# Optimization experiments

Measured on AMD Instinct MI355X. Metric: run time of the kernel, lower is better.

Reference implementation:

```python
import jax, jax.numpy as jnp
import numpy as np

N_EMBD = 1024
H_DIM = 1024
NB = 16          # blocks resolved by _find_dynamic_num_blocks for all projections
N_MEM = 128
N_FORG = H_DIM - N_MEM
RANK = 64
LOG_DT_INIT = -2.0
EPS = 1.1920929e-07  # torch fp32 finfo eps used by F.rms_norm


def rms_norm(x):
    return x * jax.lax.rsqrt(jnp.mean(jnp.square(x), axis=-1, keepdims=True) + EPS)


def silu(x):
    return x * jax.nn.sigmoid(x)


def blockdiag(x, w):
    # x: [..., nb*bi], w: [nb, bo, bi] -> [..., nb*bo]
    nb, bo, bi = w.shape
    xs = x.reshape(*x.shape[:-1], nb, bi)
    y = jnp.einsum('...ni,noi->...no', xs, w)
    return y.reshape(*x.shape[:-1], nb * bo)


def causal_scan(drive, a):
    # drive: [B,T,D] float32, a: [D] per-channel decay; causal conv with kernel a^t via FFT
    B, T, D = drive.shape
    steps = jnp.arange(T, dtype=jnp.float32)
    kernel = jnp.exp(jnp.log(jnp.maximum(a, 1e-6))[:, None] * steps[None, :])  # [D,T]
    n_fft = 1 << int(2 * T - 1).bit_length()
    df = jnp.fft.rfft(drive.astype(jnp.float32).transpose(0, 2, 1), n=n_fft, axis=-1)
    kf = jnp.fft.rfft(kernel, n=n_fft, axis=-1)
    y = jnp.fft.irfft(df * kf[None], n=n_fft, axis=-1)[..., :T]
    return y.transpose(0, 2, 1).astype(drive.dtype)


def geom_gain(a, K):
    one_minus = 1.0 - a
    safe = jnp.maximum(one_minus, 1e-8)
    return jnp.where(jnp.abs(one_minus) < 1e-6,
                     jnp.full_like(a, float(K)),
                     (1.0 - a ** K) / safe)


def setup_inputs() -> dict:
    key = jax.random.key(0)
    ks = jax.random.split(key, 10)
    s = 0.02
    bi_e, bo_h = N_EMBD // NB, H_DIM // NB
    bi_p = (2 * N_EMBD + H_DIM) // NB
    bo_e = N_EMBD // NB
    return {
        'x': jax.random.normal(ks[0], (4, 4096, N_EMBD), dtype=jnp.float32),
        'active_k': 4,
        'b_seq_w': jax.random.normal(ks[1], (NB, bo_h, bi_e), jnp.float32) * s,
        'b_depth_w': jax.random.normal(ks[2], (NB, bo_h, bi_e), jnp.float32) * s,
        'w_post_w': jax.random.normal(ks[3], (NB, bo_h, bi_p), jnp.float32) * s,
        'w_local_w': jax.random.normal(ks[4], (NB, bo_e, H_DIM // NB), jnp.float32) * s,
        'lr_A': jax.random.normal(ks[5], (N_EMBD, RANK), jnp.float32) * s,
        'lr_B': jax.random.normal(ks[6], (RANK, H_DIM), jnp.float32) * s,
        'log_A_seq': jnp.zeros((H_DIM,), jnp.float32),
        'log_dt_seq': jnp.full((H_DIM,), LOG_DT_INIT, jnp.float32),
        'log_A_depth': jnp.zeros((N_FORG,), jnp.float32),
        'log_dt_depth': jnp.full((N_FORG,), LOG_DT_INIT, jnp.float32),
    }


def reference(x, active_k, b_seq_w, b_depth_w, w_post_w, w_local_w, lr_A, lr_B,
              log_A_seq, log_dt_seq, log_A_depth, log_dt_depth):
    K = int(active_k)
    e = rms_norm(x)
    shifted_e = jnp.pad(e[:, :-1], ((0, 0), (1, 0), (0, 0)))
    a_seq = jnp.exp(-jnp.exp(log_A_seq) * jnp.exp(log_dt_seq))
    h_seq = causal_scan(silu(blockdiag(e, b_seq_w)), a_seq)
    a_forg = jnp.exp(-jnp.exp(log_A_depth) * jnp.exp(log_dt_depth))
    a_depth = jnp.concatenate([jnp.ones((N_MEM,), a_forg.dtype), a_forg], axis=0)
    gain = geom_gain(a_depth, K).astype(x.dtype)
    h_depth = gain * silu(blockdiag(e, b_depth_w))
    h = h_seq + h_depth
    r = silu(blockdiag(jnp.concatenate([rms_norm(h), e, shifted_e], axis=-1), w_post_w))
    out = x + blockdiag(r, w_local_w) + (r @ lr_B.T) @ lr_A.T
    return out
```

## Files before the change

kernel.cpp:

```cpp
#include <hip/hip_runtime.h>

#define B_ 4
#define T_ 4096
#define D_ 1024
#define R_ (B_*T_)
#define CHUNK_ 64
#define NCH_ (T_/CHUNK_)
#define EPS_ 1.1920929e-07f

typedef unsigned short ushort_t;
typedef __attribute__((ext_vector_type(8))) short short8;
typedef __attribute__((ext_vector_type(4))) float f32x4;

__device__ __forceinline__ float silu_f(float v){ return v / (1.0f + __expf(-v)); }

__device__ __forceinline__ ushort_t f2bf(float f){
    unsigned u = __float_as_uint(f);
    unsigned r = u + 0x7fffu + ((u>>16)&1u);
    return (ushort_t)(r>>16);
}
__device__ __forceinline__ float bf2f(ushort_t s){ return __uint_as_float(((unsigned)s)<<16); }

__device__ __forceinline__ f32x4 mfma16(short8 a, short8 b, f32x4 c){
    return __builtin_amdgcn_mfma_f32_16x16x32_bf16(a, b, c, 0, 0, 0);
}

__global__ void prep_k(const float* __restrict__ s0, const float* __restrict__ s1,
                       const float* __restrict__ s2, const float* __restrict__ s3,
                       const float* __restrict__ s4, const float* __restrict__ s5,
                       ushort_t* __restrict__ d0, ushort_t* __restrict__ d1,
                       ushort_t* __restrict__ d2, ushort_t* __restrict__ d3,
                       ushort_t* __restrict__ d4, ushort_t* __restrict__ d5,
                       const float* __restrict__ logA_seq, const float* __restrict__ logdt_seq,
                       const float* __restrict__ logA_dep, const float* __restrict__ logdt_dep,
                       const int* __restrict__ active_k,
                       float* __restrict__ aseq, float* __restrict__ apowC,
                       float* __restrict__ gain, float* __restrict__ apowtab){
    int i = blockIdx.x*256 + threadIdx.x;
    if      (i < 65536)   d0[i] = f2bf(s0[i]);
    else if (i < 131072)  d1[i-65536] = f2bf(s1[i-65536]);
    else if (i < 327680)  d2[i-131072] = f2bf(s2[i-131072]);
    else if (i < 393216)  d3[i-327680] = f2bf(s3[i-327680]);
    else if (i < 458752)  d4[i-393216] = f2bf(s4[i-393216]);
    else if (i < 524288)  d5[i-458752] = f2bf(s5[i-458752]);
    else if (i < 524288 + D_){
        int d = i - 524288;
        float K = (float)(*active_k);
        float a = expf(-expf(logA_seq[d]) * expf(logdt_seq[d]));
        a = fmaxf(a, 1e-6f);
        aseq[d] = a;
        apowC[d] = powf(a, (float)CHUNK_);
        float ap = a;
        for (int s2=0;s2<CHUNK_;++s2){ apowtab[s2*D_ + d] = ap; ap *= a; }
        float g;
        if (d < 128) {
            g = K;
        } else {
            float ad = expf(-expf(logA_dep[d-128]) * expf(logdt_dep[d-128]));
            float om = 1.0f - ad;
            if (fabsf(om) < 1e-6f) g = K;
            else g = (1.0f - powf(ad, K)) / fmaxf(om, 1e-8f);
        }
        gain[d] = g;
    }
}

__global__ __launch_bounds__(256) void rmsbf_k(const float* __restrict__ x, ushort_t* __restrict__ e){
    int row = blockIdx.x;
    int tid = threadIdx.x;
    float4 v = ((const float4*)(x + (size_t)row*D_))[tid];
    float ss = v.x*v.x + v.y*v.y + v.z*v.z + v.w*v.w;
    for (int off=32; off; off>>=1) ss += __shfl_down(ss, off, 64);
    __shared__ float red[4];
    if ((tid&63)==0) red[tid>>6] = ss;
    __syncthreads();
    float tot = red[0]+red[1]+red[2]+red[3];
    float scale = 1.0f / sqrtf(tot*(1.0f/D_) + EPS_);
    ushort4 o;
    o.x = f2bf(v.x*scale); o.y = f2bf(v.y*scale); o.z = f2bf(v.z*scale); o.w = f2bf(v.w*scale);
    ((ushort4*)(e + (size_t)row*D_))[tid] = o;
}

__global__ __launch_bounds__(256) void bd2s_k(const ushort_t* __restrict__ e,
        const ushort_t* __restrict__ wseq, const ushort_t* __restrict__ wdep,
        const float* __restrict__ gain, const float* __restrict__ aseq,
        ushort_t* __restrict__ hsum, float* __restrict__ carry){
    __shared__ __align__(16) ushort_t st[4][16][72];
    int wave = threadIdx.x>>6, lane = threadIdx.x&63;
    int m = lane&15, quad = lane>>4;
    int orow = lane>>2, oq = lane&3;
    int n = blockIdx.y;
    int chunk0 = blockIdx.x*256 + wave*64;

    short8 bs[2][4], bd[2][4];
    #pragma unroll
    for (int s=0;s<2;++s)
        #pragma unroll
        for (int c=0;c<4;++c){
            bs[s][c] = *(const short8*)(wseq + n*4096 + (c*16+m)*64 + s*32 + quad*8);
            bd[s][c] = *(const short8*)(wdep + n*4096 + (c*16+m)*64 + s*32 + quad*8);
        }
    float g[4], av[4], a4v[4], C[4];
    #pragma unroll
    for (int c=0;c<4;++c){
        g[c]  = gain[n*64 + c*16 + m];
        float a = aseq[n*64 + c*16 + m];
        av[c] = a;
        float a2 = a*a;
        a4v[c] = a2*a2;
        C[c] = 0.f;
    }

    #pragma unroll
    for (int t=0;t<4;++t){
        int r0 = chunk0 + t*16;
        const ushort_t* ab = e + (size_t)(r0+m)*D_ + n*64 + quad*8;
        short8 a0 = *(const short8*)ab;
        short8 a1 = *(const short8*)(ab + 32);
        f32x4 accs[4], accd[4];
        #pragma unroll
        for (int c=0;c<4;++c){
            accs[c]=(f32x4)0.f; accd[c]=(f32x4)0.f;
            accs[c]=mfma16(a0, bs[0][c], accs[c]);
            accd[c]=mfma16(a0, bd[0][c], accd[c]);
            accs[c]=mfma16(a1, bs[1][c], accs[c]);
            accd[c]=mfma16(a1, bd[1][c], accd[c]);
        }
        #pragma unroll
        for (int c=0;c<4;++c){
            float a  = av[c];
            float d0 = silu_f(accs[c][0]);
            float d1 = silu_f(accs[c][1]);
            float d2 = silu_f(accs[c][2]);
            float d3 = silu_f(accs[c][3]);
            float p1 = fmaf(a, d0, d1);
            float p2 = fmaf(a, p1, d2);
            float p3 = fmaf(a, p2, d3);
            float M = a4v[c], Bv = p3;
            float Mp = __shfl_up(M, 16, 64);
            float Bp = __shfl_up(Bv, 16, 64);
            if (quad >= 1){ Bv = fmaf(M, Bp, Bv); M *= Mp; }
            Mp = __shfl_up(M, 32, 64);
            Bp = __shfl_up(Bv, 32, 64);
            if (quad >= 2){ Bv = fmaf(M, Bp, Bv); M *= Mp; }
            float KB = __shfl_up(Bv, 16, 64);
            float KM = __shfl_up(M, 16, 64);
            float K  = (quad==0) ? C[c] : fmaf(KM, C[c], KB);
            float h0 = fmaf(a, K,  d0);
            float h1 = fmaf(a, h0, d1);
            float h2 = fmaf(a, h1, d2);
            float h3 = fmaf(a, h2, d3);
            float Cn = fmaf(M, C[c], Bv);
            C[c] = __shfl(Cn, 48 + m, 64);
            st[wave][quad*4+0][c*16+m] = f2bf(h0 + g[c]*silu_f(accd[c][0]));
            st[wave][quad*4+1][c*16+m] = f2bf(h1 + g[c]*silu_f(accd[c][1]));
            st[wave][quad*4+2][c*16+m] = f2bf(h2 + g[c]*silu_f(accd[c][2]));
            st[wave][quad*4+3][c*16+m] = f2bf(h3 + g[c]*silu_f(accd[c][3]));
        }
        ushort_t* db = hsum + (size_t)(r0+orow)*D_ + n*64;
        #pragma unroll
        for (int it=0;it<2;++it)
            *(short8*)(db + (it*4+oq)*8) = *(const short8*)&st[wave][orow][(it*4+oq)*8];
    }
    float Cv = (quad==0) ? C[0] : (quad==1) ? C[1] : (quad==2) ? C[2] : C[3];
    carry[(size_t)(chunk0>>6)*D_ + n*64 + lane] = Cv;
}

__global__ __launch_bounds__(64) void scan2_k(float* __restrict__ carry, const float* __restrict__ apowC){
    int tid = blockIdx.x*64 + threadIdx.x;
    int d = tid & (D_-1);
    int b = tid >> 10;
    float aC = apowC[d];
    float s[NCH_];
    #pragma unroll
    for (int c=0;c<NCH_;++c) s[c] = carry[(size_t)(b*NCH_+c)*D_ + d];
    float pref = 0.f;
    #pragma unroll
    for (int c=0;c<NCH_;++c){
        float cur = s[c];
        carry[(size_t)(b*NCH_+c)*D_ + d] = pref;
        pref = fmaf(aC, pref, cur);
    }
}

__global__ __launch_bounds__(256) void scan3s_k(const ushort_t* __restrict__ hsum,
                                                const float* __restrict__ aseq,
                                                const float* __restrict__ carry,
                                                const float* __restrict__ apowtab,
                                                ushort_t* __restrict__ hn){
    __shared__ float part[4][4];
    __shared__ float scl[8];
    int tid = threadIdx.x;
    int lane = tid & 63, wave = tid >> 6;
    int cg = tid & 127;
    int rp = tid >> 7;
    int d0 = cg*8;
    int row0 = blockIdx.x*8;
    int bc = row0 >> 6;
    int s0 = row0 & 63;

    float a2[8], P[8], apow[8];
    #pragma unroll
    for (int j=0;j<8;++j){
        float aj = aseq[d0+j];
        a2[j] = aj*aj;
        P[j]  = carry[(size_t)bc*D_ + d0 + j];
        apow[j] = apowtab[(size_t)(s0 + rp)*D_ + d0 + j];
    }

    float hf[4][8];
    #pragma unroll
    for (int i=0;i<4;++i){
        int row = row0 + i*2 + rp;
        short8 v = *(const short8*)(hsum + (size_t)row*D_ + d0);
        float ss = 0.f;
        #pragma unroll
        for (int j=0;j<8;++j){
            float f = bf2f((ushort_t)v[j]) + P[j]*apow[j];
            hf[i][j] = f;
            ss += f*f;
            apow[j] *= a2[j];
        }
        for (int off=32; off; off>>=1) ss += __shfl_down(ss, off, 64);
        if (lane==0) part[wave][i] = ss;
    }
    __syncthreads();
    if (tid < 8){
        int r = tid;
        int rr = r & 1, ii = r >> 1;
        float sum = part[rr*2][ii] + part[rr*2+1][ii];
        scl[r] = rsqrtf(sum*(1.0f/D_) + EPS_);
    }
    __syncthreads();
    #pragma unroll
    for (int i=0;i<4;++i){
        int rloc = i*2 + rp;
        float sc = scl[rloc];
        short8 o;
        #pragma unroll
        for (int j=0;j<8;++j) o[j] = (short)f2bf(hf[i][j]*sc);
        *(short8*)(hn + (size_t)(row0 + rloc)*D_ + d0) = o;
    }
}

__global__ __launch_bounds__(256) void post_k(const ushort_t* __restrict__ hn,
                                              const ushort_t* __restrict__ e,
                                              const ushort_t* __restrict__ wpost, ushort_t* __restrict__ rout){
    __shared__ __align__(16) ushort_t st[4][16][72];
    int wave = threadIdx.x>>6, lane = threadIdx.x&63;
    int m = lane&15, quad = lane>>4;
    int orow = lane>>2, oq = lane&3;
    int n = blockIdx.y;
    int row0 = blockIdx.x*128 + wave*32 + m;

    f32x4 acc[2][4];
    #pragma unroll
    for (int t=0;t<2;++t)
        #pragma unroll
        for (int c=0;c<4;++c) acc[t][c]=(f32x4)0.f;

    #pragma unroll 1
    for (int s=0;s<6;++s){
        int g0 = n*192 + s*32;
        short8 bw[4];
        #pragma unroll
        for (int c=0;c<4;++c)
            bw[c] = *(const short8*)(wpost + n*(64*192) + (c*16+m)*192 + s*32 + quad*8);
        #pragma unroll
        for (int t=0;t<2;++t){
            int row = row0 + t*16;
            short8 af;
            if (g0 < 1024){
                af = *(const short8*)(hn + (size_t)row*D_ + g0 + quad*8);
            } else if (g0 < 2048){
                af = *(const short8*)(e + (size_t)row*D_ + (g0-1024) + quad*8);
            } else {
                if ((row & (T_-1)) == 0) af = short8{0,0,0,0,0,0,0,0};
                else af = *(const short8*)(e + (size_t)(row-1)*D_ + (g0-2048) + quad*8);
            }
            #pragma unroll
            for (int c=0;c<4;++c)
                acc[t][c] = mfma16(af, bw[c], acc[t][c]);
        }
    }
    #pragma unroll
    for (int t=0;t<2;++t){
        int r0 = blockIdx.x*128 + wave*32 + t*16;
        #pragma unroll
        for (int c=0;c<4;++c)
            #pragma unroll
            for (int r=0;r<4;++r)
                st[wave][quad*4+r][c*16+m] = f2bf(silu_f(acc[t][c][r]));
        ushort_t* db = rout + (size_t)(r0+orow)*D_ + n*64;
        #pragma unroll
        for (int it=0;it<2;++it)
            *(short8*)(db + (it*4+oq)*8) = *(const short8*)&st[wave][orow][(it*4+oq)*8];
    }
}

__global__ __launch_bounds__(256) void rlow_k(const ushort_t* __restrict__ r, const ushort_t* __restrict__ lrB,
                                              ushort_t* __restrict__ rlow){
    __shared__ __align__(16) float sacc[4][16][68];
    int wave = threadIdx.x>>6, lane = threadIdx.x&63;
    int m = lane&15, quad = lane>>4;
    int r0 = blockIdx.x*16;
    f32x4 acc[4];
    #pragma unroll
    for (int c=0;c<4;++c) acc[c]=(f32x4)0.f;
    const ushort_t* ab = r + (size_t)(r0+m)*D_ + wave*256 + quad*8;
    #pragma unroll
    for (int s=0;s<8;++s){
        short8 a = *(const short8*)(ab + s*32);
        #pragma unroll
        for (int c=0;c<4;++c){
            short8 b = *(const short8*)(lrB + (c*16+m)*1024 + wave*256 + s*32 + quad*8);
            acc[c] = mfma16(a, b, acc[c]);
        }
    }
    #pragma unroll
    for (int c=0;c<4;++c)
        #pragma unroll
        for (int r2=0;r2<4;++r2)
            sacc[wave][quad*4+r2][c*16+m] = acc[c][r2];
    __syncthreads();
    int row  = threadIdx.x>>4;
    int col4 = (threadIdx.x&15)*4;
    float4 v0 = *(const float4*)&sacc[0][row][col4];
    float4 v1 = *(const float4*)&sacc[1][row][col4];
    float4 v2 = *(const float4*)&sacc[2][row][col4];
    float4 v3 = *(const float4*)&sacc[3][row][col4];
    ushort4 o;
    o.x = f2bf(v0.x+v1.x+v2.x+v3.x);
    o.y = f2bf(v0.y+v1.y+v2.y+v3.y);
    o.z = f2bf(v0.z+v1.z+v2.z+v3.z);
    o.w = f2bf(v0.w+v1.w+v2.w+v3.w);
    *(ushort4*)(rlow + (size_t)(r0+row)*64 + col4) = o;
}

__global__ __launch_bounds__(256) void out_k(const float* __restrict__ x, const ushort_t* __restrict__ r,
        const ushort_t* __restrict__ rlow, const ushort_t* __restrict__ wloc, const ushort_t* __restrict__ lrA,
        float* __restrict__ out){
    __shared__ __align__(16) float st[4][16][68];
    int wave = threadIdx.x>>6, lane = threadIdx.x&63;
    int m = lane&15, quad = lane>>4;
    int orow = lane>>2, oq = lane&3;
    int n = blockIdx.y;

    short8 wl[2][4], la[4][2];
    #pragma unroll
    for (int c=0;c<4;++c)
        #pragma unroll
        for (int s=0;s<2;++s){
            wl[s][c] = *(const short8*)(wloc + n*4096 + (c*16+m)*64 + s*32 + quad*8);
            la[c][s] = *(const short8*)(lrA + (size_t)(n*64 + c*16 + m)*64 + s*32 + quad*8);
        }
    #pragma unroll
    for (int t=0;t<2;++t){
        int r0 = blockIdx.x*128 + wave*32 + t*16;
        const float* xb = x + (size_t)(r0+orow)*D_ + n*64;
        float4 xv[4];
        #pragma unroll
        for (int it=0;it<4;++it) xv[it] = *(const float4*)(xb + (it*4+oq)*4);

        const ushort_t* lb = rlow + (size_t)(r0+m)*64 + quad*8;
        short8 al0 = *(const short8*)lb;
        short8 al1 = *(const short8*)(lb + 32);
        const ushort_t* ab = r + (size_t)(r0+m)*D_ + n*64 + quad*8;
        short8 ar0 = *(const short8*)ab;
        short8 ar1 = *(const short8*)(ab + 32);
        f32x4 acc[4];
        #pragma unroll
        for (int c=0;c<4;++c){
            acc[c]=(f32x4)0.f;
            acc[c]=mfma16(al0, la[c][0], acc[c]);
            acc[c]=mfma16(al1, la[c][1], acc[c]);
            acc[c]=mfma16(ar0, wl[0][c], acc[c]);
            acc[c]=mfma16(ar1, wl[1][c], acc[c]);
        }
        #pragma unroll
        for (int c=0;c<4;++c)
            #pragma unroll
            for (int r2=0;r2<4;++r2)
                st[wave][quad*4+r2][c*16+m] = acc[c][r2];
        float* ob = out + (size_t)(r0+orow)*D_ + n*64;
        #pragma unroll
        for (int it=0;it<4;++it){
            float4 v = *(const float4*)&st[wave][orow][(it*4+oq)*4];
            v.x += xv[it].x; v.y += xv[it].y; v.z += xv[it].z; v.w += xv[it].w;
            *(float4*)(ob + (it*4+oq)*4) = v;
        }
    }
}

extern "C" void kernel_launch(void* const* d_in, const int* in_sizes, int n_in,
                              void* d_out, int out_size, void* d_ws, size_t ws_size,
                              hipStream_t stream) {
    const float* x         = (const float*)d_in[0];
    const int*   active_k  = (const int*)  d_in[1];
    const float* b_seq_w   = (const float*)d_in[2];
    const float* b_depth_w = (const float*)d_in[3];
    const float* w_post_w  = (const float*)d_in[4];
    const float* w_local_w = (const float*)d_in[5];
    const float* lr_A      = (const float*)d_in[6];
    const float* lr_B      = (const float*)d_in[7];
    const float* logA_seq  = (const float*)d_in[8];
    const float* logdt_seq = (const float*)d_in[9];
    const float* logA_dep  = (const float*)d_in[10];
    const float* logdt_dep = (const float*)d_in[11];

    float* ws      = (float*)d_ws;
    float* carry   = ws;
    float* aseq    = carry + (size_t)B_*NCH_*D_;
    float* apowC   = aseq + D_;
    float* gain    = apowC + D_;
    float* apowtab = gain + D_;
    ushort_t* ub       = (ushort_t*)(apowtab + (size_t)CHUNK_*D_);
    ushort_t* e_bf     = ub;
    ushort_t* hsum_bf  = e_bf + (size_t)R_*D_;
    ushort_t* hn_bf    = hsum_bf + (size_t)R_*D_;
    ushort_t* r_bf     = hn_bf + (size_t)R_*D_;
    ushort_t* rlow_bf  = r_bf + (size_t)R_*D_;
    ushort_t* wseq_bf  = rlow_bf + (size_t)R_*64;
    ushort_t* wdep_bf  = wseq_bf + 65536;
    ushort_t* wpost_bf = wdep_bf + 65536;
    ushort_t* wloc_bf  = wpost_bf + 196608;
    ushort_t* lrA_bf   = wloc_bf + 65536;
    ushort_t* lrB_bf   = lrA_bf + 65536;

    prep_k<<<(524288 + D_ + 255)/256, 256, 0, stream>>>(
        b_seq_w, b_depth_w, w_post_w, w_local_w, lr_A, lr_B,
        wseq_bf, wdep_bf, wpost_bf, wloc_bf, lrA_bf, lrB_bf,
        logA_seq, logdt_seq, logA_dep, logdt_dep, active_k, aseq, apowC, gain, apowtab);

    rmsbf_k <<<R_, 256, 0, stream>>>(x, e_bf);
    bd2s_k  <<<dim3(R_/256, 16), 256, 0, stream>>>(e_bf, wseq_bf, wdep_bf, gain, aseq,
                                                   hsum_bf, carry);
    scan2_k <<<(B_*D_)/64, 64, 0, stream>>>(carry, apowC);
    scan3s_k<<<R_/8, 256, 0, stream>>>(hsum_bf, aseq, carry, apowtab, hn_bf);
    post_k  <<<dim3(R_/128, 16), 256, 0, stream>>>(hn_bf, e_bf, wpost_bf, r_bf);
    rlow_k  <<<R_/16, 256, 0, stream>>>(r_bf, lrB_bf, rlow_bf);
    out_k   <<<dim3(R_/128, 16), 256, 0, stream>>>(x, r_bf, rlow_bf, wloc_bf, lrA_bf, (float*)d_out);
}
```

Baseline: 271.3 us.

## Stage post_k weights in LDS and prefetch activations via global_load_lds

```diff
diff --git a/kernel.cpp b/kernel.cpp
--- a/kernel.cpp
+++ b/kernel.cpp
@@ -11,6 +11,8 @@
 typedef unsigned short ushort_t;
 typedef __attribute__((ext_vector_type(8))) short short8;
 typedef __attribute__((ext_vector_type(4))) float f32x4;
+typedef __attribute__((address_space(1))) ushort_t gu16;
+typedef __attribute__((address_space(3))) ushort_t lu16;
 
 __device__ __forceinline__ float silu_f(float v){ return v / (1.0f + __expf(-v)); }
 
@@ -246,38 +248,66 @@
 __global__ __launch_bounds__(256) void post_k(const ushort_t* __restrict__ hn,
                                               const ushort_t* __restrict__ e,
                                               const ushort_t* __restrict__ wpost, ushort_t* __restrict__ rout){
-    __shared__ __align__(16) ushort_t st[4][16][72];
+    __shared__ __align__(16) ushort_t stage[4][6144];
+    __shared__ __align__(16) ushort_t wlds[64*208];
     int wave = threadIdx.x>>6, lane = threadIdx.x&63;
     int m = lane&15, quad = lane>>4;
     int orow = lane>>2, oq = lane&3;
     int n = blockIdx.y;
     int row0 = blockIdx.x*128 + wave*32 + m;
-
-    f32x4 acc[2][4];
-    #pragma unroll
-    for (int t=0;t<2;++t)
-        #pragma unroll
-        for (int c=0;c<4;++c) acc[t][c]=(f32x4)0.f;
-
-    #pragma unroll 1
+    ushort_t* wst = &stage[wave][0];
+
+    {
+        const ushort_t* wsrc = wpost + n*(64*192);
+        int tid = threadIdx.x;
+        #pragma unroll
+        for (int k=0;k<6;++k){
+            int chunk = tid + k*256;
+            int rr = chunk / 24, cc = chunk % 24;
+            *(short8*)(wlds + rr*208 + cc*8) = *(const short8*)(wsrc + rr*192 + cc*8);
+        }
+    }
+    __syncthreads();
+
+    #pragma unroll
     for (int s=0;s<6;++s){
         int g0 = n*192 + s*32;
-        short8 bw[4];
-        #pragma unroll
-        for (int c=0;c<4;++c)
-            bw[c] = *(const short8*)(wpost + n*(64*192) + (c*16+m)*192 + s*32 + quad*8);
         #pragma unroll
         for (int t=0;t<2;++t){
             int row = row0 + t*16;
-            short8 af;
-            if (g0 < 1024){
-                af = *(const short8*)(hn + (size_t)row*D_ + g0 + quad*8);
-            } else if (g0 < 2048){
-                af = *(const short8*)(e + (size_t)row*D_ + (g0-1024) + quad*8);
-            } else {
-                if ((row & (T_-1)) == 0) af = short8{0,0,0,0,0,0,0,0};
-                else af = *(const short8*)(e + (size_t)(row-1)*D_ + (g0-2048) + quad*8);
-            }
+            const ushort_t* src;
+            if (g0 < 1024)      src = hn + (size_t)row*D_ + g0 + quad*8;
+            else if (g0 < 2048) src = e + (size_t)row*D_ + (g0-1024) + quad*8;
+            else                src = e + (size_t)(row-1)*D_ + (g0-2048) + quad*8;
+            __builtin_amdgcn_global_load_lds((const gu16*)src, (lu16*)(wst + (s*2+t)*512), 16, 0, 0);
+        }
+    }
+
+    f32x4 acc[2][4];
+    #pragma unroll
+    for (int t=0;t<2;++t)
+        #pragma unroll
+        for (int c=0;c<4;++c) acc[t][c]=(f32x4)0.f;
+
+    #pragma unroll
+    for (int s=0;s<6;++s){
+        if      (s==0) asm volatile("s_waitcnt vmcnt(10)" ::: "memory");
+        else if (s==1) asm volatile("s_waitcnt vmcnt(8)"  ::: "memory");
+        else if (s==2) asm volatile("s_waitcnt vmcnt(6)"  ::: "memory");
+        else if (s==3) asm volatile("s_waitcnt vmcnt(4)"  ::: "memory");
+        else if (s==4) asm volatile("s_waitcnt vmcnt(2)"  ::: "memory");
+        else           asm volatile("s_waitcnt vmcnt(0)"  ::: "memory");
+        __builtin_amdgcn_sched_barrier(0);
+        int g0 = n*192 + s*32;
+        short8 bw[4];
+        #pragma unroll
+        for (int c=0;c<4;++c)
+            bw[c] = *(const short8*)(wlds + (c*16+m)*208 + s*32 + quad*8);
+        #pragma unroll
+        for (int t=0;t<2;++t){
+            short8 af = *(const short8*)(wst + (s*2+t)*512 + lane*8);
+            int row = row0 + t*16;
+            if (g0 >= 2048 && ((row & (T_-1)) == 0)) af = short8{0,0,0,0,0,0,0,0};
             #pragma unroll
             for (int c=0;c<4;++c)
                 acc[t][c] = mfma16(af, bw[c], acc[t][c]);
@@ -290,11 +320,11 @@
         for (int c=0;c<4;++c)
             #pragma unroll
             for (int r=0;r<4;++r)
-                st[wave][quad*4+r][c*16+m] = f2bf(silu_f(acc[t][c][r]));
+                wst[(quad*4+r)*72 + c*16+m] = f2bf(silu_f(acc[t][c][r]));
         ushort_t* db = rout + (size_t)(r0+orow)*D_ + n*64;
         #pragma unroll
         for (int it=0;it<2;++it)
-            *(short8*)(db + (it*4+oq)*8) = *(const short8*)&st[wave][orow][(it*4+oq)*8];
+            *(short8*)(db + (it*4+oq)*8) = *(const short8*)&wst[orow*72 + (it*4+oq)*8];
     }
 }
 
```

Result: faster. 261.1 us, median of 2 (-3.8%).
